# Kernel tuning notes

Hardware: AMD Instinct MI355X
Metric: run time of the kernel (lower is better)

Reference implementation:

```python
import jax, jax.numpy as jnp
import numpy as np

B, CIN, COUT, COFF, H, W = 4, 256, 256, 256, 64, 64
DG, K = 16, 3            # deformable groups, kernel size
KK = K * K               # 9 taps


def _conv3x3(x, w, b):
    y = jax.lax.conv_general_dilated(x, w, window_strides=(1, 1), padding='SAME',
                                     dimension_numbers=('NCHW', 'OIHW', 'NCHW'))
    return y + b[None, :, None, None]


def _bilinear_sample(xg, ys, xs):
    # xg: [B,DG,Cg,H,W]; ys,xs: [B,DG,Ho,Wo] float sampling coords (zero padding outside)
    Bn, dg, Cg, Hh, Ww = xg.shape
    xf = xg.reshape(Bn, dg, Cg, Hh * Ww)
    y0 = jnp.floor(ys)
    x0 = jnp.floor(xs)
    wy = (ys - y0)[:, :, None]  # [B,DG,1,Ho,Wo]
    wx = (xs - x0)[:, :, None]

    def gather(yi, xi):
        valid = (yi >= 0) & (yi < Hh) & (xi >= 0) & (xi < Ww)
        yc = jnp.clip(yi, 0, Hh - 1).astype(jnp.int32)
        xc = jnp.clip(xi, 0, Ww - 1).astype(jnp.int32)
        idx = (yc * Ww + xc).reshape(Bn, dg, 1, -1)
        v = jnp.take_along_axis(xf, jnp.broadcast_to(idx, (Bn, dg, Cg, idx.shape[-1])), axis=-1)
        v = v.reshape(Bn, dg, Cg, ys.shape[2], ys.shape[3])
        return v * valid[:, :, None].astype(xg.dtype)

    v00 = gather(y0, x0)
    v01 = gather(y0, x0 + 1)
    v10 = gather(y0 + 1, x0)
    v11 = gather(y0 + 1, x0 + 1)
    return v00 * (1 - wy) * (1 - wx) + v01 * (1 - wy) * wx + v10 * wy * (1 - wx) + v11 * wy * wx


def _deform_conv2d(x, offset, mask, weight, bias):
    # torchvision modulated deform_conv2d, stride=1, padding=1, dilation=1, groups=1
    Bn, C, Hh, Ww = x.shape
    Cg = C // DG
    xg = x.reshape(Bn, DG, Cg, Hh, Ww)
    # offset channel layout: 2*(g*KK + k) -> dy, +1 -> dx
    off = offset.reshape(Bn, DG, KK, 2, Hh, Ww)
    msk = mask.reshape(Bn, DG, KK, Hh, Ww)
    wk = weight.reshape(weight.shape[0], DG, Cg, K, K)
    hb = jnp.arange(Hh, dtype=x.dtype)[:, None]
    wb = jnp.arange(Ww, dtype=x.dtype)[None, :]
    acc = jnp.zeros((Bn, weight.shape[0], Hh, Ww), dtype=x.dtype)
    for ki in range(K):
        for kj in range(K):
            k = ki * K + kj
            ys = hb - 1 + ki + off[:, :, k, 0]   # padding=1, dilation=1
            xs = wb - 1 + kj + off[:, :, k, 1]
            s = _bilinear_sample(xg, ys, xs) * msk[:, :, k][:, :, None]  # [B,DG,Cg,H,W]
            acc = acc + jnp.einsum('bgchw,ogc->bohw', s, wk[:, :, :, ki, kj])
    return acc + bias[None, :, None, None]


def setup_inputs() -> dict:
    key = jax.random.key(0)
    ks = jax.random.split(key, 10)
    s = 0.02
    return {
        'x': jax.random.normal(ks[0], (B, CIN, H, W), jnp.float32),
        'offset_feat': jax.random.normal(ks[1], (B, COFF, H, W), jnp.float32),
        'weight': jax.random.normal(ks[2], (COUT, CIN, K, K), jnp.float32) * s,
        'bias': jax.random.normal(ks[3], (COUT,), jnp.float32) * s,
        'w1': jax.random.normal(ks[4], (COUT, COFF, K, K), jnp.float32) * s,
        'b1': jax.random.normal(ks[5], (COUT,), jnp.float32) * s,
        'w2': jax.random.normal(ks[6], (COUT, COUT, K, K), jnp.float32) * s,
        'b2': jax.random.normal(ks[7], (COUT,), jnp.float32) * s,
        'w3': jax.random.normal(ks[8], (27 * DG, COUT, K, K), jnp.float32) * 0.01,
        'b3': jax.random.normal(ks[9], (27 * DG,), jnp.float32) * 0.01,
    }


def reference(x, offset_feat, weight, bias, w1, b1, w2, b2, w3, b3):
    out = jax.nn.silu(_conv3x3(offset_feat, w1, b1))
    out = jax.nn.silu(_conv3x3(out, w2, b2))
    out = _conv3x3(out, w3, b3)                 # [B, 27*DG, H, W]
    o1, o2, m = jnp.split(out, 3, axis=1)
    offset = jnp.concatenate([o1, o2], axis=1)  # [B, 2*DG*9, H, W]
    mask = jax.nn.sigmoid(m)                    # [B, DG*9, H, W]
    return _deform_conv2d(x, offset, mask, weight, bias)
```

## Files before the change

kernel.cpp:

```cpp
#include <hip/hip_runtime.h>
#include <math.h>

typedef __attribute__((ext_vector_type(8))) short  bf16x8;
typedef __attribute__((ext_vector_type(8))) unsigned short u16x8;
typedef __attribute__((ext_vector_type(4))) float  f32x4;

#define MTOT 16384

__device__ __forceinline__ float b2f(unsigned short h) {
  return __uint_as_float(((unsigned int)h) << 16);
}
__device__ __forceinline__ unsigned short f2bf(float f) {
  unsigned int u = __float_as_uint(f);
  unsigned int r = (u + 0x7fffu + ((u >> 16) & 1u)) >> 16;
  return (unsigned short)r;
}
__device__ __forceinline__ void gload16(const unsigned short* g, unsigned short* l) {
  __builtin_amdgcn_global_load_lds(
      (const __attribute__((address_space(1))) void*)g,
      (__attribute__((address_space(3))) void*)l, 16, 0, 0);
}

__global__ __launch_bounds__(256) void nhwc_kernel(const float* __restrict__ in,
                                                   unsigned short* __restrict__ out) {
  const int y = blockIdx.x, b = blockIdx.y;
  const int t = threadIdx.x;
  __shared__ float lds[64 * 65];
  for (int c0 = 0; c0 < 256; c0 += 64) {
    #pragma unroll
    for (int i = 0; i < 16; ++i) {
      int cl = i * 4 + (t >> 6);
      int xx = t & 63;
      lds[cl * 65 + xx] = in[(((size_t)b * 256 + c0 + cl) * 64 + y) * 64 + xx];
    }
    __syncthreads();
    const int plane = c0 >> 6;
    #pragma unroll
    for (int i = 0; i < 16; ++i) {
      int xx = i * 4 + (t >> 6);
      int cl = t & 63;
      int m  = (b << 12) + (y << 6) + xx;
      out[((size_t)plane * MTOT + m) * 64 + cl] = f2bf(lds[cl * 65 + xx]);
    }
    __syncthreads();
  }
}

__global__ __launch_bounds__(256) void wprep_kernel(const float* __restrict__ w,
                                                    unsigned short* __restrict__ Wp,
                                                    int COUT_valid) {
  const int kkc4 = blockIdx.x;
  const int kk = kkc4 >> 2, c4 = kkc4 & 3;
  const int co = blockIdx.y * 4 + (threadIdx.x >> 6);
  const int c16 = threadIdx.x & 63;
  float v = (co < COUT_valid) ? w[((size_t)co * 256 + c4 * 64 + c16) * 9 + kk] : 0.0f;
  Wp[((size_t)kkc4 * 512 + co) * 64 + c16] = f2bf(v);
}

__global__ __launch_bounds__(256) void sampler_kernel(const float* __restrict__ t3,
                                                      const unsigned short* __restrict__ xh,
                                                      unsigned short* __restrict__ S) {
  const int t = threadIdx.x;
  const int h = t & 1;
  const int g = (t >> 1) & 15;
  const int m = blockIdx.x * 8 + (t >> 5);
  const int b = m >> 12, pix = m & 4095, y = pix >> 6, x = pix & 63;
  const float* off = t3 + (size_t)m * 432;
  const size_t gbase = ((size_t)(g >> 2) * MTOT + ((size_t)b << 12)) * 64 + (g & 3) * 16 + h * 8;

  #pragma unroll
  for (int kk = 0; kk < 9; ++kk) {
    const int ki = kk / 3, kj = kk % 3;
    float dyv = off[2 * (g * 9 + kk)];
    float dxv = off[2 * (g * 9 + kk) + 1];
    float ml  = off[288 + g * 9 + kk];
    float mk  = 1.0f / (1.0f + __expf(-ml));
    float ysf = (float)(y - 1 + ki) + dyv;
    float xsf = (float)(x - 1 + kj) + dxv;
    float y0f = floorf(ysf), x0f = floorf(xsf);
    float wy = ysf - y0f, wx = xsf - x0f;
    int yi0 = (int)y0f, xi0 = (int)x0f;
    int yi1 = yi0 + 1, xi1 = xi0 + 1;
    bool vy0 = (yi0 >= 0) && (yi0 < 64), vy1 = (yi1 >= 0) && (yi1 < 64);
    bool vx0 = (xi0 >= 0) && (xi0 < 64), vx1 = (xi1 >= 0) && (xi1 < 64);
    int yc0 = min(max(yi0, 0), 63), yc1 = min(max(yi1, 0), 63);
    int xc0 = min(max(xi0, 0), 63), xc1 = min(max(xi1, 0), 63);
    float w00 = (vy0 && vx0) ? (1.f - wy) * (1.f - wx) * mk : 0.f;
    float w01 = (vy0 && vx1) ? (1.f - wy) * wx * mk : 0.f;
    float w10 = (vy1 && vx0) ? wy * (1.f - wx) * mk : 0.f;
    float w11 = (vy1 && vx1) ? wy * wx * mk : 0.f;

    const int p00 = yc0 * 64 + xc0, p01 = yc0 * 64 + xc1;
    const int p10 = yc1 * 64 + xc0, p11 = yc1 * 64 + xc1;
    u16x8 c00 = *(const u16x8*)(xh + gbase + (size_t)p00 * 64);
    u16x8 c01 = *(const u16x8*)(xh + gbase + (size_t)p01 * 64);
    u16x8 c10 = *(const u16x8*)(xh + gbase + (size_t)p10 * 64);
    u16x8 c11 = *(const u16x8*)(xh + gbase + (size_t)p11 * 64);
    u16x8 o;
    #pragma unroll
    for (int j = 0; j < 8; ++j) {
      float s = w00 * b2f(c00[j]) + w01 * b2f(c01[j]) + w10 * b2f(c10[j]) + w11 * b2f(c11[j]);
      o[j] = f2bf(s);
    }
    *(u16x8*)(S + ((size_t)(kk * 4 + (g >> 2)) * MTOT + m) * 64 + (g & 3) * 16 + h * 8) = o;
  }
}

template<int EPI, bool IMPLICIT>
__global__ __launch_bounds__(512, 1) void gemmC_kernel(
    const unsigned short* __restrict__ A,
    const unsigned short* __restrict__ W,
    const float* __restrict__ bias,
    void* __restrict__ outp,
    const unsigned short* __restrict__ zbuf,
    int Nvalid) {
  constexpr int BM = 128, BN = 128, BK = 64, NSTEP = 36, NPAD = 512;
  __shared__ unsigned short lds[2][(BM + BN) * BK];

  const int t = threadIdx.x, lane = t & 63, w = t >> 6;
  const int wm = w >> 2, wn = w & 3;
  const int m0 = blockIdx.x * BM, n0 = blockIdx.y * BN;

  const unsigned short* baseA[2];
  const unsigned short* zsrcA[2];
  unsigned int vmaskA[2];
  #pragma unroll
  for (int i = 0; i < 2; ++i) {
    int c   = (i * 8 + w) * 64 + lane;
    int row = c >> 3;
    int ccl = (c & 7) ^ (row & 7);
    int m   = m0 + row;
    baseA[i] = A + (size_t)m * 64 + ccl * 8;
    zsrcA[i] = zbuf + ccl * 8;
    if (IMPLICIT) {
      int y = (m >> 6) & 63, x = m & 63;
      unsigned int vm = 0;
      #pragma unroll
      for (int kk = 0; kk < 9; ++kk) {
        int dy = kk / 3 - 1, dx = kk % 3 - 1;
        if ((unsigned)(y + dy) < 64u && (unsigned)(x + dx) < 64u) vm |= (1u << kk);
      }
      vmaskA[i] = vm;
    } else {
      vmaskA[i] = 0;
    }
  }
  const unsigned short* baseB[2];
  #pragma unroll
  for (int j = 0; j < 2; ++j) {
    int c   = (j * 8 + w) * 64 + lane;
    int row = c >> 3;
    int ccl = (c & 7) ^ (row & 7);
    baseB[j] = W + (size_t)(n0 + row) * 64 + ccl * 8;
  }

  int offA[4][2], offB[2][2];
  #pragma unroll
  for (int mi = 0; mi < 4; ++mi) {
    int r = wm * 64 + mi * 16 + (lane & 15);
    #pragma unroll
    for (int kh = 0; kh < 2; ++kh)
      offA[mi][kh] = r * 64 + (((kh * 4 + (lane >> 4)) ^ (r & 7)) * 8);
  }
  #pragma unroll
  for (int nj = 0; nj < 2; ++nj) {
    int r = wn * 32 + nj * 16 + (lane & 15);
    #pragma unroll
    for (int kh = 0; kh < 2; ++kh)
      offB[nj][kh] = BM * BK + r * 64 + (((kh * 4 + (lane >> 4)) ^ (r & 7)) * 8);
  }

  f32x4 acc[4][2];
  #pragma unroll
  for (int mi = 0; mi < 4; ++mi)
    #pragma unroll
    for (int nj = 0; nj < 2; ++nj) acc[mi][nj] = (f32x4){0.f, 0.f, 0.f, 0.f};

  auto STAGE = [&](int sn, unsigned short* buf) {
    const long boff = (long)sn * (NPAD * 64);
    if (IMPLICIT) {
      int kkn = sn >> 2;
      int q3  = kkn / 3;
      const long aoff = (long)(sn & 3) * (MTOT * 64) + (long)((q3 - 1) * 64 + (kkn - q3 * 3 - 1)) * 64;
      #pragma unroll
      for (int i = 0; i < 2; ++i) {
        const unsigned short* src = ((vmaskA[i] >> kkn) & 1u) ? baseA[i] + aoff : zsrcA[i];
        gload16(src, buf + (i * 8 + w) * 512);
      }
    } else {
      const long aoff = (long)sn * (MTOT * 64);
      #pragma unroll
      for (int i = 0; i < 2; ++i)
        gload16(baseA[i] + aoff, buf + (i * 8 + w) * 512);
    }
    #pragma unroll
    for (int j = 0; j < 2; ++j)
      gload16(baseB[j] + boff, buf + BM * BK + (j * 8 + w) * 512);
  };

  STAGE(0, lds[0]);

  for (int s = 0; s < NSTEP; ++s) {
    if (s + 1 < NSTEP) {
      STAGE(s + 1, lds[(s + 1) & 1]);
      asm volatile("s_waitcnt vmcnt(4)" ::: "memory");
    } else {
      asm volatile("s_waitcnt vmcnt(0)" ::: "memory");
    }
    __builtin_amdgcn_s_barrier();
    __builtin_amdgcn_sched_barrier(0);

    const unsigned short* cb = lds[s & 1];
    bf16x8 af[4][2], bfg[2][2];
    #pragma unroll
    for (int mi = 0; mi < 4; ++mi)
      #pragma unroll
      for (int kh = 0; kh < 2; ++kh)
        af[mi][kh] = *(const bf16x8*)&cb[offA[mi][kh]];
    #pragma unroll
    for (int nj = 0; nj < 2; ++nj)
      #pragma unroll
      for (int kh = 0; kh < 2; ++kh)
        bfg[nj][kh] = *(const bf16x8*)&cb[offB[nj][kh]];

    #pragma unroll
    for (int kh = 0; kh < 2; ++kh)
      #pragma unroll
      for (int mi = 0; mi < 4; ++mi)
        #pragma unroll
        for (int nj = 0; nj < 2; ++nj)
          acc[mi][nj] = __builtin_amdgcn_mfma_f32_16x16x32_bf16(af[mi][kh], bfg[nj][kh],
                                                                acc[mi][nj], 0, 0, 0);
    __builtin_amdgcn_sched_barrier(0);
    asm volatile("s_waitcnt lgkmcnt(0)" ::: "memory");
    __builtin_amdgcn_s_barrier();
  }

  const int gmBase = m0 + wm * 64 + (lane >> 4) * 4;
  const int gnBase = n0 + wn * 32 + (lane & 15);
  #pragma unroll
  for (int nj = 0; nj < 2; ++nj) {
    const int gn = gnBase + nj * 16;
    const bool nv = (gn < Nvalid);
    const float bv = nv ? bias[gn] : 0.f;
    #pragma unroll
    for (int mi = 0; mi < 4; ++mi) {
      #pragma unroll
      for (int r = 0; r < 4; ++r) {
        const int gm = gmBase + mi * 16 + r;
        float v = acc[mi][nj][r] + bv;
        if (EPI == 0) {
          if (nv) {
            float sv = v / (1.0f + __expf(-v));
            ((unsigned short*)outp)[((size_t)(gn >> 6) * MTOT + gm) * 64 + (gn & 63)] = f2bf(sv);
          }
        } else if (EPI == 1) {
          if (nv) ((float*)outp)[(size_t)gm * 432 + gn] = v;
        } else {
          if (nv) ((float*)outp)[((size_t)(gm >> 12) * 256 + gn) * 4096 + (gm & 4095)] = v;
        }
      }
    }
  }
}

extern "C" void kernel_launch(void* const* d_in, const int* in_sizes, int n_in,
                              void* d_out, int out_size, void* d_ws, size_t ws_size,
                              hipStream_t stream) {
  const float* x      = (const float*)d_in[0];
  const float* offeat = (const float*)d_in[1];
  const float* weight = (const float*)d_in[2];
  const float* bias   = (const float*)d_in[3];
  const float* w1     = (const float*)d_in[4];
  const float* b1     = (const float*)d_in[5];
  const float* w2     = (const float*)d_in[6];
  const float* b2     = (const float*)d_in[7];
  const float* w3     = (const float*)d_in[8];
  const float* b3     = (const float*)d_in[9];
  float* out = (float*)d_out;

  char* ws = (char*)d_ws;
  unsigned short* xh  = (unsigned short*)(ws + 0);
  float*          t3  = (float*)(ws + 8388608);
  unsigned short* Wd  = (unsigned short*)(ws + 36700160);
  unsigned short* zb  = (unsigned short*)(ws + 39059456);
  unsigned short* S   = (unsigned short*)(ws + 39059712);
  unsigned short* fh  = (unsigned short*)(ws + 39059712);
  unsigned short* t1  = (unsigned short*)(ws + 47448320);
  unsigned short* t2  = (unsigned short*)(ws + 55836928);
  unsigned short* W1p = (unsigned short*)(ws + 64225536);
  unsigned short* W2p = (unsigned short*)(ws + 66584832);
  unsigned short* W3p = (unsigned short*)(ws + 68944128);

  hipMemsetAsync(zb, 0, 256, stream);

  nhwc_kernel<<<dim3(64, 4), 256, 0, stream>>>(x, xh);
  nhwc_kernel<<<dim3(64, 4), 256, 0, stream>>>(offeat, fh);
  wprep_kernel<<<dim3(36, 128), 256, 0, stream>>>(w1, W1p, 256);
  wprep_kernel<<<dim3(36, 128), 256, 0, stream>>>(w2, W2p, 256);
  wprep_kernel<<<dim3(36, 128), 256, 0, stream>>>(w3, W3p, 432);
  wprep_kernel<<<dim3(36, 128), 256, 0, stream>>>(weight, Wd, 256);

  gemmC_kernel<0, true ><<<dim3(128, 4), 512, 0, stream>>>(fh, W1p, b1, t1, zb, 256);
  gemmC_kernel<0, true ><<<dim3(128, 4), 512, 0, stream>>>(t1, W2p, b2, t2, zb, 256);
  gemmC_kernel<1, true ><<<dim3(128, 4), 512, 0, stream>>>(t2, W3p, b3, t3, zb, 432);

  sampler_kernel<<<dim3(2048), 256, 0, stream>>>(t3, xh, S);

  gemmC_kernel<2, false><<<dim3(128, 4), 512, 0, stream>>>(S, Wd, bias, out, zb, 256);
}
```

Before: 226.0 us.

## Split-K the 256-channel GEMMs with bf16 partials and separate reduce kernels

Replaces the first two offset-branch convolutions and the final deform GEMM with a split-K kernel that uses 128x128 tiles and a grid of 128x2x4 blocks. It writes bf16 partial sums to a workspace buffer, and separate reduce kernels then add the bias and apply SiLU or the NCHW output transpose. The aim is more blocks in flight and better MFMA tile reuse than the earlier 512-thread launches with only 512 blocks. The cost is extra global traffic for the partials, two extra launches, and bf16 rounding of the partial sums. The deform split only runs if the workspace is large enough and otherwise falls back to the old kernel.

```diff
diff --git a/kernel.cpp b/kernel.cpp
--- a/kernel.cpp
+++ b/kernel.cpp
@@ -249,12 +249,7 @@
       for (int r = 0; r < 4; ++r) {
         const int gm = gmBase + mi * 16 + r;
         float v = acc[mi][nj][r] + bv;
-        if (EPI == 0) {
-          if (nv) {
-            float sv = v / (1.0f + __expf(-v));
-            ((unsigned short*)outp)[((size_t)(gn >> 6) * MTOT + gm) * 64 + (gn & 63)] = f2bf(sv);
-          }
-        } else if (EPI == 1) {
+        if (EPI == 1) {
           if (nv) ((float*)outp)[(size_t)gm * 432 + gn] = v;
         } else {
           if (nv) ((float*)outp)[((size_t)(gm >> 12) * 256 + gn) * 4096 + (gm & 4095)] = v;
@@ -262,6 +257,193 @@
       }
     }
   }
+}
+
+template<bool IMPLICIT>
+__global__ __launch_bounds__(256, 4) void gemmS_kernel(
+    const unsigned short* __restrict__ A,
+    const unsigned short* __restrict__ W,
+    unsigned short* __restrict__ P,
+    const unsigned short* __restrict__ zbuf) {
+  constexpr int NSTEP = 18;
+  __shared__ unsigned short lds[2][8192];
+
+  const int t = threadIdx.x, lane = t & 63, w = t >> 6;
+  const int wm = w >> 1, wn = w & 1;
+  const int m0 = blockIdx.x * 128, n0 = blockIdx.y * 128;
+  const int ks = blockIdx.z, gs0 = ks * NSTEP;
+
+  const unsigned short* baseA[2];
+  const unsigned short* zsrcA[2];
+  unsigned int vmaskA[2];
+  #pragma unroll
+  for (int i = 0; i < 2; ++i) {
+    int c    = (i * 4 + w) * 64 + lane;
+    int line = c >> 3;
+    int ccl  = (c & 7) ^ (line & 7);
+    int m    = m0 + line * 2 + (ccl >> 2);
+    baseA[i] = A + (size_t)m * 64 + (ccl & 3) * 8;
+    zsrcA[i] = zbuf + (ccl & 3) * 8;
+    if (IMPLICIT) {
+      int y = (m >> 6) & 63, x = m & 63;
+      unsigned int vm = 0;
+      #pragma unroll
+      for (int kk = 0; kk < 9; ++kk) {
+        int dy = kk / 3 - 1, dx = kk % 3 - 1;
+        if ((unsigned)(y + dy) < 64u && (unsigned)(x + dx) < 64u) vm |= (1u << kk);
+      }
+      vmaskA[i] = vm;
+    } else {
+      vmaskA[i] = 0;
+    }
+  }
+  const unsigned short* baseB[2];
+  #pragma unroll
+  for (int j = 0; j < 2; ++j) {
+    int c    = (j * 4 + w) * 64 + lane;
+    int line = c >> 3;
+    int ccl  = (c & 7) ^ (line & 7);
+    int co   = n0 + line * 2 + (ccl >> 2);
+    baseB[j] = W + (size_t)co * 64 + (ccl & 3) * 8;
+  }
+
+  int offA[4], offB[4];
+  #pragma unroll
+  for (int mi = 0; mi < 4; ++mi) {
+    int row  = wm * 64 + mi * 16 + (lane & 15);
+    int line = row >> 1;
+    int pos  = (row & 1) * 4 + (lane >> 4);
+    offA[mi] = line * 64 + ((pos ^ (line & 7)) * 8);
+  }
+  #pragma unroll
+  for (int nj = 0; nj < 4; ++nj) {
+    int row  = wn * 64 + nj * 16 + (lane & 15);
+    int line = row >> 1;
+    int pos  = (row & 1) * 4 + (lane >> 4);
+    offB[nj] = 4096 + line * 64 + ((pos ^ (line & 7)) * 8);
+  }
+
+  f32x4 acc[4][4];
+  #pragma unroll
+  for (int mi = 0; mi < 4; ++mi)
+    #pragma unroll
+    for (int nj = 0; nj < 4; ++nj) acc[mi][nj] = (f32x4){0.f, 0.f, 0.f, 0.f};
+
+  auto STAGE = [&](int s, unsigned short* buf) {
+    const int gs = gs0 + s;
+    const int half32 = (gs & 1) * 32;
+    const long boff = (long)(gs >> 1) * (512 * 64) + half32;
+    if (IMPLICIT) {
+      int kkn = gs >> 3;
+      int q3  = kkn / 3;
+      const long shift = (long)((q3 - 1) * 64 + (kkn - q3 * 3 - 1));
+      const long aoff = ((long)((gs & 7) >> 1) * MTOT + shift) * 64 + half32;
+      #pragma unroll
+      for (int i = 0; i < 2; ++i) {
+        const unsigned short* src = ((vmaskA[i] >> kkn) & 1u) ? baseA[i] + aoff : zsrcA[i];
+        gload16(src, buf + (i * 4 + w) * 512);
+      }
+    } else {
+      const long aoff = (long)(gs >> 1) * (MTOT * 64) + half32;
+      #pragma unroll
+      for (int i = 0; i < 2; ++i)
+        gload16(baseA[i] + aoff, buf + (i * 4 + w) * 512);
+    }
+    #pragma unroll
+    for (int j = 0; j < 2; ++j)
+      gload16(baseB[j] + boff, buf + 4096 + (j * 4 + w) * 512);
+  };
+
+  STAGE(0, lds[0]);
+
+  for (int s = 0; s < NSTEP; ++s) {
+    if (s + 1 < NSTEP) {
+      STAGE(s + 1, lds[(s + 1) & 1]);
+      asm volatile("s_waitcnt vmcnt(4)" ::: "memory");
+    } else {
+      asm volatile("s_waitcnt vmcnt(0)" ::: "memory");
+    }
+    __builtin_amdgcn_s_barrier();
+    __builtin_amdgcn_sched_barrier(0);
+
+    const unsigned short* cb = lds[s & 1];
+    bf16x8 af[4], bfg[4];
+    #pragma unroll
+    for (int mi = 0; mi < 4; ++mi) af[mi] = *(const bf16x8*)&cb[offA[mi]];
+    #pragma unroll
+    for (int nj = 0; nj < 4; ++nj) bfg[nj] = *(const bf16x8*)&cb[offB[nj]];
+
+    #pragma unroll
+    for (int mi = 0; mi < 4; ++mi)
+      #pragma unroll
+      for (int nj = 0; nj < 4; ++nj)
+        acc[mi][nj] = __builtin_amdgcn_mfma_f32_16x16x32_bf16(af[mi], bfg[nj],
+                                                              acc[mi][nj], 0, 0, 0);
+    __builtin_amdgcn_sched_barrier(0);
+    asm volatile("s_waitcnt lgkmcnt(0)" ::: "memory");
+    __builtin_amdgcn_s_barrier();
+  }
+
+  unsigned short* pk = P + (size_t)ks * (MTOT * 256);
+  const int gmBase = m0 + wm * 64 + (lane >> 4) * 4;
+  const int gnBase = n0 + wn * 64 + (lane & 15);
+  #pragma unroll
+  for (int nj = 0; nj < 4; ++nj) {
+    const int gn = gnBase + nj * 16;
+    #pragma unroll
+    for (int mi = 0; mi < 4; ++mi) {
+      #pragma unroll
+      for (int r = 0; r < 4; ++r) {
+        const int gm = gmBase + mi * 16 + r;
+        pk[(size_t)gm * 256 + gn] = f2bf(acc[mi][nj][r]);
+      }
+    }
+  }
+}
+
+__global__ __launch_bounds__(256) void reduce_silu_kernel(
+    const unsigned short* __restrict__ P, const float* __restrict__ bias,
+    unsigned short* __restrict__ out) {
+  const int idx = blockIdx.x * 256 + threadIdx.x;
+  const size_t v8 = (size_t)idx * 8;
+  const int m = (int)(v8 >> 8), ch0 = (int)(v8 & 255);
+  float s[8];
+  #pragma unroll
+  for (int j = 0; j < 8; ++j) s[j] = bias[ch0 + j];
+  #pragma unroll
+  for (int ks = 0; ks < 4; ++ks) {
+    u16x8 p = *(const u16x8*)(P + (size_t)ks * (MTOT * 256) + v8);
+    #pragma unroll
+    for (int j = 0; j < 8; ++j) s[j] += b2f(p[j]);
+  }
+  u16x8 o;
+  #pragma unroll
+  for (int j = 0; j < 8; ++j) {
+    float v = s[j];
+    o[j] = f2bf(v / (1.0f + __expf(-v)));
+  }
+  *(u16x8*)(out + ((size_t)(ch0 >> 6) * MTOT + m) * 64 + (ch0 & 63)) = o;
+}
+
+__global__ __launch_bounds__(256) void reduce_out_kernel(
+    const unsigned short* __restrict__ P, const float* __restrict__ bias,
+    float* __restrict__ out) {
+  const int idx = blockIdx.x * 256 + threadIdx.x;
+  const size_t v8 = (size_t)idx * 8;
+  const int m = (int)(v8 >> 8), ch0 = (int)(v8 & 255);
+  float s[8];
+  #pragma unroll
+  for (int j = 0; j < 8; ++j) s[j] = bias[ch0 + j];
+  #pragma unroll
+  for (int ks = 0; ks < 4; ++ks) {
+    u16x8 p = *(const u16x8*)(P + (size_t)ks * (MTOT * 256) + v8);
+    #pragma unroll
+    for (int j = 0; j < 8; ++j) s[j] += b2f(p[j]);
+  }
+  const int b = m >> 12, pix = m & 4095;
+  #pragma unroll
+  for (int j = 0; j < 8; ++j)
+    out[((size_t)b * 256 + ch0 + j) * 4096 + pix] = s[j];
 }
 
 extern "C" void kernel_launch(void* const* d_in, const int* in_sizes, int n_in,
@@ -291,6 +473,11 @@
   unsigned short* W1p = (unsigned short*)(ws + 64225536);
   unsigned short* W2p = (unsigned short*)(ws + 66584832);
   unsigned short* W3p = (unsigned short*)(ws + 68944128);
+  unsigned short* P1  = (unsigned short*)(ws + 71303424);
+  const size_t P2_OFF  = 114557184;
+  const size_t NEED_P2 = P2_OFF + 33554432;
+  unsigned short* P2  = (unsigned short*)(ws + P2_OFF);
+  const bool split_deform = (ws_size >= NEED_P2);
 
   hipMemsetAsync(zb, 0, 256, stream);
 
@@ -301,11 +488,20 @@
   wprep_kernel<<<dim3(36, 128), 256, 0, stream>>>(w3, W3p, 432);
   wprep_kernel<<<dim3(36, 128), 256, 0, stream>>>(weight, Wd, 256);
 
-  gemmC_kernel<0, true ><<<dim3(128, 4), 512, 0, stream>>>(fh, W1p, b1, t1, zb, 256);
-  gemmC_kernel<0, true ><<<dim3(128, 4), 512, 0, stream>>>(t1, W2p, b2, t2, zb, 256);
-  gemmC_kernel<1, true ><<<dim3(128, 4), 512, 0, stream>>>(t2, W3p, b3, t3, zb, 432);
+  gemmS_kernel<true><<<dim3(128, 2, 4), 256, 0, stream>>>(fh, W1p, P1, zb);
+  reduce_silu_kernel<<<dim3(2048), 256, 0, stream>>>(P1, b1, t1);
+
+  gemmS_kernel<true><<<dim3(128, 2, 4), 256, 0, stream>>>(t1, W2p, P1, zb);
+  reduce_silu_kernel<<<dim3(2048), 256, 0, stream>>>(P1, b2, t2);
+
+  gemmC_kernel<1, true><<<dim3(128, 4), 512, 0, stream>>>(t2, W3p, b3, t3, zb, 432);
 
   sampler_kernel<<<dim3(2048), 256, 0, stream>>>(t3, xh, S);
 
-  gemmC_kernel<2, false><<<dim3(128, 4), 512, 0, stream>>>(S, Wd, bias, out, zb, 256);
-}
+  if (split_deform) {
+    gemmS_kernel<false><<<dim3(128, 2, 4), 256, 0, stream>>>(S, Wd, P2, zb);
+    reduce_out_kernel<<<dim3(2048), 256, 0, stream>>>(P2, bias, out);
+  } else {
+    gemmC_kernel<2, false><<<dim3(128, 4), 512, 0, stream>>>(S, Wd, bias, out, zb, 256);
+  }
+}
```

Result: slower. 230.6 us (+2.0%).
